# Kernel optimization log

Hardware: AMD Instinct MI355X
Metric: run time of the kernel (lower is better)

The kernel has to match this reference:

```python
import jax, jax.numpy as jnp
import numpy as np

D, H = 1024, 2048
N_STEPS = 2
T0, T1 = 0.0, 1.0


def setup_inputs() -> dict:
    key = jax.random.key(0)
    ks = jax.random.split(key, 5)
    s_in = 1.0 / np.sqrt(D)
    s_h = 1.0 / np.sqrt(H)
    return {
        "x0": jax.random.normal(ks[0], (D,), jnp.float32),
        "W1": jax.random.normal(ks[1], (D, H), jnp.float32) * s_in,
        "b1": jnp.zeros((H,), jnp.float32),
        "wt": jax.random.normal(ks[2], (H,), jnp.float32) * 0.1,
        "W2": jax.random.normal(ks[3], (H, H), jnp.float32) * s_h,
        "b2": jnp.zeros((H,), jnp.float32),
        "W3": jax.random.normal(ks[4], (H, D), jnp.float32) * s_h,
        "b3": jnp.zeros((D,), jnp.float32),
    }


def reference(x0, W1, b1, wt, W2, b2, W3, b3):
    dtype = x0.dtype

    def velocity(t, x):
        # 3-layer tanh MLP velocity field with additive time embedding
        h1 = jnp.tanh(x @ W1 + b1 + t * wt)
        h2 = jnp.tanh(h1 @ W2 + b2)
        return h2 @ W3 + b3

    def vel_and_div(t, x):
        # Mirror of _compute_velocity_and_divergence: linearize + vmap(jvp)
        # over identity to get the full Jacobian, then take its trace.
        v, jvp_fun = jax.linearize(lambda z: velocity(t, z), x)
        cols = jax.vmap(jvp_fun)(jnp.eye(D, dtype=dtype))  # [D, D]
        return v, jnp.trace(cols)

    def aug_dyn(t, x):
        v, div = vel_and_div(t, x)
        return v, -div  # (dx/dt, dlogq/dt)

    # Standard-normal base distribution log_prob at x0
    log2pi = jnp.log(jnp.asarray(2.0 * np.pi, dtype=dtype))
    logq0 = -0.5 * jnp.sum(x0 * x0) - 0.5 * D * log2pi

    dt = jnp.asarray((T1 - T0) / N_STEPS, dtype=dtype)

    def rk4_step(carry, i):
        x, logq = carry
        t = T0 + i * dt
        v1, dl1 = aug_dyn(t, x)
        v2, dl2 = aug_dyn(t + 0.5 * dt, x + 0.5 * dt * v1)
        v3, dl3 = aug_dyn(t + 0.5 * dt, x + 0.5 * dt * v2)
        v4, dl4 = aug_dyn(t + dt, x + dt * v3)
        x_new = x + (dt / 6.0) * (v1 + 2.0 * v2 + 2.0 * v3 + v4)
        logq_new = logq + (dt / 6.0) * (dl1 + 2.0 * dl2 + 2.0 * dl3 + dl4)
        return (x_new, logq_new), None

    (x1, logq1), _ = jax.lax.scan(
        rk4_step, (x0, logq0), jnp.arange(N_STEPS, dtype=dtype)
    )
    # concat [x1 (D,), logq1 ()] -> (D+1,) for a single output array
    return jnp.concatenate([x1, logq1[None]])
```

## Files before the change

### kernel.cpp

```cpp
#include <hip/hip_runtime.h>
#include <math.h>

#define DD 1024
#define HH 2048
#define NCB 256

typedef float f32x4 __attribute__((ext_vector_type(4)));
typedef short short8 __attribute__((ext_vector_type(8)));

__device__ __forceinline__ float b2f(unsigned short u) {
    return __uint_as_float(((unsigned int)u) << 16);
}
__device__ __forceinline__ unsigned short f2b(float f) {
    unsigned int x = __float_as_uint(f);
    unsigned int r = (x + 0x7FFFu + ((x >> 16) & 1u)) >> 16;
    return (unsigned short)r;
}
__device__ __forceinline__ float ald(const float* p) {
    return __hip_atomic_load(p, __ATOMIC_RELAXED, __HIP_MEMORY_SCOPE_AGENT);
}
__device__ __forceinline__ void ast(float* p, float v) {
    __hip_atomic_store(p, v, __ATOMIC_RELAXED, __HIP_MEMORY_SCOPE_AGENT);
}

__global__ __launch_bounds__(256) void k_preW1(const float* __restrict__ W1,
                                               unsigned short* __restrict__ W1T,
                                               unsigned* __restrict__ sync) {
    __shared__ float tile[64][65];
    const int b = blockIdx.x, t = threadIdx.x;
    if (b == 0) {
        #pragma unroll
        for (int q = 0; q < 19; ++q) {
            int i = t + q * 256;
            if (i < 4624) sync[i] = 0u;
        }
    }
    const int bx = b & 31, by = b >> 5;
    const int c0 = bx * 64, r0 = by * 64;
    const int cc = t & 63, rb = t >> 6;
    #pragma unroll
    for (int p = 0; p < 16; ++p) {
        int rr = p * 4 + rb;
        tile[rr][cc] = W1[(size_t)(r0 + rr) * HH + c0 + cc];
    }
    __syncthreads();
    #pragma unroll
    for (int p = 0; p < 16; ++p) {
        int rr = p * 4 + rb;
        W1T[(size_t)(c0 + rr) * DD + r0 + cc] = f2b(tile[cc][rr]);
    }
}

__global__ __launch_bounds__(256) void k_gemmPT(const unsigned short* __restrict__ W1T,
                                                const float* __restrict__ W2,
                                                const float* __restrict__ W3,
                                                const float* __restrict__ b3,
                                                const float* __restrict__ x0,
                                                unsigned short* __restrict__ Mb,
                                                unsigned short* __restrict__ Pb,
                                                unsigned short* __restrict__ W2T,
                                                unsigned short* __restrict__ W3T,
                                                float* __restrict__ c1,
                                                float* __restrict__ A1g) {
    const int b = blockIdx.x, t = threadIdx.x;
    if (b >= 256) {
        __shared__ float tile[64][65];
        int bb = b - 256;
        const float* in; unsigned short* out; int R, C, bx, by;
        if (bb < 1024) { in = W2; out = W2T; R = HH; C = HH; bx = bb & 31; by = bb >> 5; }
        else           { bb -= 1024; in = W3; out = W3T; R = HH; C = DD; bx = bb & 15; by = bb >> 4; }
        const int c0 = bx * 64, r0 = by * 64;
        const int cc = t & 63, rb = t >> 6;
        #pragma unroll
        for (int p = 0; p < 16; ++p) {
            int rr = p * 4 + rb;
            tile[rr][cc] = in[(size_t)(r0 + rr) * C + c0 + cc];
        }
        __syncthreads();
        #pragma unroll
        for (int p = 0; p < 16; ++p) {
            int rr = p * 4 + rb;
            out[(size_t)(c0 + rr) * R + r0 + cc] = f2b(tile[cc][rr]);
        }
        return;
    }
    __shared__ unsigned short At[128][40];
    __shared__ unsigned short Bt[128][40];
    const int m0 = (b >> 4) * 128;
    const int k0 = (b & 15) * 128;
    const int r = t & 127, half = t >> 7;
    const int wv = t >> 6, l = t & 63;
    const int wr = wv >> 1, wc = wv & 1;
    const int fr = l & 15, fg = l >> 4;
    const bool do_c1 = ((b & 15) == 0) && (t < 128);
    float c1acc = 0.f, a1acc = 0.f;

    f32x4 acc[4][4] = {};
    for (int i0 = 0; i0 < DD; i0 += 32) {
        {
            const float4* sa = (const float4*)(W1T + (size_t)(m0 + r) * DD + i0 + half * 16);
            float4 a0 = sa[0], a1 = sa[1];
            const float4* sbf = (const float4*)(W3 + (size_t)(k0 + r) * DD + i0 + half * 16);
            float4 f0 = sbf[0], f1 = sbf[1], f2v = sbf[2], f3 = sbf[3];
            float4* da = (float4*)&At[r][half * 16];
            da[0] = a0; da[1] = a1;
            short8 o0, o1;
            o0[0] = (short)f2b(f0.x); o0[1] = (short)f2b(f0.y); o0[2] = (short)f2b(f0.z); o0[3] = (short)f2b(f0.w);
            o0[4] = (short)f2b(f1.x); o0[5] = (short)f2b(f1.y); o0[6] = (short)f2b(f1.z); o0[7] = (short)f2b(f1.w);
            o1[0] = (short)f2b(f2v.x); o1[1] = (short)f2b(f2v.y); o1[2] = (short)f2b(f2v.z); o1[3] = (short)f2b(f2v.w);
            o1[4] = (short)f2b(f3.x); o1[5] = (short)f2b(f3.y); o1[6] = (short)f2b(f3.z); o1[7] = (short)f2b(f3.w);
            *(short8*)&Bt[r][half * 16] = o0;
            *(short8*)&Bt[r][half * 16 + 8] = o1;
        }
        __syncthreads();
        if (do_c1) {
            #pragma unroll
            for (int i = 0; i < 32; ++i) {
                float w1v = b2f(At[t][i]);
                c1acc += w1v * b3[i0 + i];
                a1acc += w1v * x0[i0 + i];
            }
        }
        short8 af[4], bf[4];
        #pragma unroll
        for (int a = 0; a < 4; ++a)
            af[a] = *(const short8*)&At[wr * 64 + a * 16 + fr][fg * 8];
        #pragma unroll
        for (int bq = 0; bq < 4; ++bq)
            bf[bq] = *(const short8*)&Bt[wc * 64 + bq * 16 + fr][fg * 8];
        #pragma unroll
        for (int a = 0; a < 4; ++a)
            #pragma unroll
            for (int bq = 0; bq < 4; ++bq)
                acc[a][bq] = __builtin_amdgcn_mfma_f32_16x16x32_bf16(af[a], bf[bq], acc[a][bq], 0, 0, 0);
        __syncthreads();
    }
    if (do_c1) { c1[m0 + t] = c1acc; A1g[m0 + t] = a1acc; }
    #pragma unroll
    for (int a = 0; a < 4; ++a) {
        #pragma unroll
        for (int bq = 0; bq < 4; ++bq) {
            #pragma unroll
            for (int j = 0; j < 4; ++j) {
                int row = m0 + wr * 64 + a * 16 + fg * 4 + j;
                int col = k0 + wc * 64 + bq * 16 + fr;
                size_t idx = (size_t)row * HH + col;
                float m = acc[a][bq][j];
                Mb[idx] = f2b(m);
                Pb[idx] = f2b(m * W2[idx]);
            }
        }
    }
}

__device__ __forceinline__ void gbar(unsigned* sync, int b, unsigned g) {
    __syncthreads();
    const int t = threadIdx.x;
    if (b == 0 && t >= 64 && t < 128) {
        const int l = t - 64;
        while (true) {
            bool ok = true;
            #pragma unroll
            for (int k = 0; k < 4; ++k) {
                unsigned f = __hip_atomic_load(&sync[(l + (k << 6)) << 4],
                                               __ATOMIC_RELAXED, __HIP_MEMORY_SCOPE_AGENT);
                ok &= (f >= g);
            }
            if (!__any((int)(!ok))) break;
            __builtin_amdgcn_s_sleep(1);
        }
        if (l < 16)
            __hip_atomic_store(&sync[4096 + (l << 4)], g, __ATOMIC_RELAXED, __HIP_MEMORY_SCOPE_AGENT);
    }
    if (t == 0) {
        asm volatile("s_waitcnt vmcnt(0)" ::: "memory");
        __hip_atomic_store(&sync[b << 4], g, __ATOMIC_RELAXED, __HIP_MEMORY_SCOPE_AGENT);
        while (__hip_atomic_load(&sync[4096 + ((b & 15) << 4)],
                                 __ATOMIC_RELAXED, __HIP_MEMORY_SCOPE_AGENT) < g)
            __builtin_amdgcn_s_sleep(2);
    }
    __syncthreads();
}

__global__ __launch_bounds__(256, 1) void k_chain(
    const unsigned short* __restrict__ Mb,
    const unsigned short* __restrict__ Pb,
    const unsigned short* __restrict__ W2T,
    const unsigned short* __restrict__ W3T,
    const float* __restrict__ x0,
    const float* __restrict__ b1, const float* __restrict__ wt,
    const float* __restrict__ b2, const float* __restrict__ b3,
    const float* __restrict__ c1, const float* __restrict__ A1g,
    float* __restrict__ h1_g, float* __restrict__ h2_g, float* __restrict__ hacc_g,
    float* __restrict__ out,
    unsigned* __restrict__ sync) {
    __shared__ unsigned short Ms[8][2048];
    __shared__ unsigned short Ps[8][2048];
    __shared__ unsigned short Qs[8][2048];
    __shared__ float vecH[2048];
    __shared__ float vecW[2048];
    __shared__ float wred[4];
    const int t = threadIdx.x, b = blockIdx.x;
    const int wib = t >> 6, lane = t & 63;
    const int gw2 = (b << 3) + (wib << 1);
    const int jx = (b << 2) + wib;
    unsigned g = 0;

    {
        const unsigned short* mp = Mb + (size_t)gw2 * HH;
        const unsigned short* pp = Pb + (size_t)gw2 * HH;
        const unsigned short* qp = W2T + (size_t)gw2 * HH;
        #pragma unroll
        for (int rep = 0; rep < 4; ++rep) {
            const int idx = rep * 512 + lane * 8;
            *(short8*)&Ms[wib * 2][idx]     = *(const short8*)(mp + idx);
            *(short8*)&Ms[wib * 2 + 1][idx] = *(const short8*)(mp + HH + idx);
            *(short8*)&Ps[wib * 2][idx]     = *(const short8*)(pp + idx);
            *(short8*)&Ps[wib * 2 + 1][idx] = *(const short8*)(pp + HH + idx);
            *(short8*)&Qs[wib * 2][idx]     = *(const short8*)(qp + idx);
            *(short8*)&Qs[wib * 2 + 1][idx] = *(const short8*)(qp + HH + idx);
        }
    }

    const float bb1_0 = b1[gw2], bb1_1 = b1[gw2 + 1];
    const float wt_0 = wt[gw2], wt_1 = wt[gw2 + 1];
    const float bb2_0 = b2[gw2], bb2_1 = b2[gw2 + 1];
    const float c1_0 = c1[gw2], c1_1 = c1[gw2 + 1];

    float A1_0 = 0.f, A1_1 = 0.f;
    float u0 = 0.f, u1 = 0.f;
    float hc0 = 0.f, hc1 = 0.f;
    float wdiv = 0.f;

    float logq_r = 0.f;
    if (b == 0 && wib == 0) {
        float ssum = 0.f;
        #pragma unroll
        for (int q = 0; q < 16; ++q) { float xv = x0[lane + (q << 6)]; ssum += xv * xv; }
        #pragma unroll
        for (int o = 1; o < 64; o <<= 1) ssum += __shfl_xor(ssum, o, 64);
        logq_r = -0.5f * ssum - 0.5f * 1024.0f * 1.8378770664093453f;
    }

    for (int s = 0; s < 8; ++s) {
        const int ss = s & 3;
        const float tcur = (s >> 2) * 0.5f + ((ss == 0) ? 0.f : (ss == 3) ? 0.5f : 0.25f);

        if (s == 0) {
            A1_0 = A1g[gw2]; A1_1 = A1g[gw2 + 1];
            float h0 = tanhf(A1_0 + bb1_0 + tcur * wt_0);
            float h1v = tanhf(A1_1 + bb1_1 + tcur * wt_1);
            u0 = 1.f - h0 * h0; u1 = 1.f - h1v * h1v;
            if (lane == 0) { ast(h1_g + gw2, h0); ast(h1_g + gw2 + 1, h1v); }
        } else {
            #pragma unroll
            for (int q = 0; q < 8; ++q) {
                int i = t + (q << 8);
                float h2v = ald(h2_g + i);
                float sv = (ss == 0) ? ald(hacc_g + i) : h2v;
                vecH[i] = sv;
                vecW[i] = 1.f - h2v * h2v;
            }
            __syncthreads();
            float md0 = 0.f, md1 = 0.f, pd0 = 0.f, pd1 = 0.f;
            #pragma unroll
            for (int rep = 0; rep < 4; ++rep) {
                const int idx = rep * 512 + lane * 8;
                float4 hA = *(const float4*)(vecH + idx);
                float4 hB = *(const float4*)(vecH + idx + 4);
                float4 wA = *(const float4*)(vecW + idx);
                float4 wB = *(const float4*)(vecW + idx + 4);
                float hv[8] = {hA.x, hA.y, hA.z, hA.w, hB.x, hB.y, hB.z, hB.w};
                float wv[8] = {wA.x, wA.y, wA.z, wA.w, wB.x, wB.y, wB.z, wB.w};
                short8 m0v = *(const short8*)&Ms[wib * 2][idx];
                short8 m1v = *(const short8*)&Ms[wib * 2 + 1][idx];
                short8 p0v = *(const short8*)&Ps[wib * 2][idx];
                short8 p1v = *(const short8*)&Ps[wib * 2 + 1][idx];
                #pragma unroll
                for (int e = 0; e < 8; ++e) {
                    md0 += b2f((unsigned short)m0v[e]) * hv[e];
                    md1 += b2f((unsigned short)m1v[e]) * hv[e];
                    pd0 += b2f((unsigned short)p0v[e]) * wv[e];
                    pd1 += b2f((unsigned short)p1v[e]) * wv[e];
                }
            }
            #pragma unroll
            for (int o = 1; o < 64; o <<= 1) {
                md0 += __shfl_xor(md0, o, 64); md1 += __shfl_xor(md1, o, 64);
                pd0 += __shfl_xor(pd0, o, 64); pd1 += __shfl_xor(pd1, o, 64);
            }
            const int sp = (s - 1) & 3;
            const float cprev = (sp == 1 || sp == 2) ? (1.f / 6.f) : (1.f / 12.f);
            wdiv += cprev * (u0 * pd0 + u1 * pd1);
            float pre0, pre1;
            if (ss == 0) {
                A1_0 += md0 + 0.5f * c1_0; A1_1 += md1 + 0.5f * c1_1;
                pre0 = A1_0 + bb1_0 + tcur * wt_0; pre1 = A1_1 + bb1_1 + tcur * wt_1;
            } else {
                const float a = (ss == 3) ? 0.5f : 0.25f;
                pre0 = A1_0 + a * (md0 + c1_0) + bb1_0 + tcur * wt_0;
                pre1 = A1_1 + a * (md1 + c1_1) + bb1_1 + tcur * wt_1;
            }
            float h0 = tanhf(pre0), h1v = tanhf(pre1);
            u0 = 1.f - h0 * h0; u1 = 1.f - h1v * h1v;
            if (lane == 0) { ast(h1_g + gw2, h0); ast(h1_g + gw2 + 1, h1v); }
        }
        gbar(sync, b, ++g);

        #pragma unroll
        for (int q = 0; q < 8; ++q) {
            int i = t + (q << 8);
            vecH[i] = ald(h1_g + i);
        }
        __syncthreads();
        {
            float a0 = 0.f, a1 = 0.f;
            #pragma unroll
            for (int rep = 0; rep < 4; ++rep) {
                const int idx = rep * 512 + lane * 8;
                float4 hA = *(const float4*)(vecH + idx);
                float4 hB = *(const float4*)(vecH + idx + 4);
                float hv[8] = {hA.x, hA.y, hA.z, hA.w, hB.x, hB.y, hB.z, hB.w};
                short8 r0 = *(const short8*)&Qs[wib * 2][idx];
                short8 r1 = *(const short8*)&Qs[wib * 2 + 1][idx];
                #pragma unroll
                for (int e = 0; e < 8; ++e) {
                    a0 += b2f((unsigned short)r0[e]) * hv[e];
                    a1 += b2f((unsigned short)r1[e]) * hv[e];
                }
            }
            #pragma unroll
            for (int o = 1; o < 64; o <<= 1) {
                a0 += __shfl_xor(a0, o, 64); a1 += __shfl_xor(a1, o, 64);
            }
            float q0 = tanhf(a0 + bb2_0), q1 = tanhf(a1 + bb2_1);
            const float cs = (ss == 1 || ss == 2) ? (1.f / 6.f) : (1.f / 12.f);
            hc0 += cs * q0; hc1 += cs * q1;
            if (lane == 0) {
                ast(h2_g + gw2, q0); ast(h2_g + gw2 + 1, q1);
                if (ss == 3) { ast(hacc_g + gw2, hc0); ast(hacc_g + gw2 + 1, hc1); }
            }
        }
        gbar(sync, b, ++g);
    }

    {
        #pragma unroll
        for (int q = 0; q < 8; ++q) {
            int i = t + (q << 8);
            float h2v = ald(h2_g + i);
            vecH[i] = ald(hacc_g + i);
            vecW[i] = 1.f - h2v * h2v;
        }
        __syncthreads();
        float pd0 = 0.f, pd1 = 0.f, xo = 0.f;
        const unsigned short* Vr = W3T + (size_t)jx * HH;
        #pragma unroll
        for (int rep = 0; rep < 4; ++rep) {
            const int idx = rep * 512 + lane * 8;
            float4 cA = *(const float4*)(vecH + idx);
            float4 cB = *(const float4*)(vecH + idx + 4);
            float4 wA = *(const float4*)(vecW + idx);
            float4 wB = *(const float4*)(vecW + idx + 4);
            float cv[8] = {cA.x, cA.y, cA.z, cA.w, cB.x, cB.y, cB.z, cB.w};
            float wv[8] = {wA.x, wA.y, wA.z, wA.w, wB.x, wB.y, wB.z, wB.w};
            short8 p0v = *(const short8*)&Ps[wib * 2][idx];
            short8 p1v = *(const short8*)&Ps[wib * 2 + 1][idx];
            short8 vv = *(const short8*)(Vr + idx);
            #pragma unroll
            for (int e = 0; e < 8; ++e) {
                pd0 += b2f((unsigned short)p0v[e]) * wv[e];
                pd1 += b2f((unsigned short)p1v[e]) * wv[e];
                xo  += b2f((unsigned short)vv[e]) * cv[e];
            }
        }
        #pragma unroll
        for (int o = 1; o < 64; o <<= 1) {
            pd0 += __shfl_xor(pd0, o, 64); pd1 += __shfl_xor(pd1, o, 64);
            xo += __shfl_xor(xo, o, 64);
        }
        wdiv += (1.f / 12.f) * (u0 * pd0 + u1 * pd1);
        if (lane == 0) {
            out[jx] = x0[jx] + xo + b3[jx];
            wred[wib] = wdiv;
        }
    }
    __syncthreads();
    if (t == 0) {
        float dsum = wred[0] + wred[1] + wred[2] + wred[3];
        atomicAdd((float*)(sync + 4352 + (b & 15) * 16), dsum);
        asm volatile("s_waitcnt vmcnt(0)" ::: "memory");
        atomicAdd(sync + 4608, 1u);
    }
    if (b == 0 && wib == 0) {
        if (lane < 16) {
            while (__hip_atomic_load(sync + 4608, __ATOMIC_RELAXED, __HIP_MEMORY_SCOPE_AGENT) < NCB)
                __builtin_amdgcn_s_sleep(2);
        }
        float v = 0.f;
        if (lane < 16) {
            unsigned du = __hip_atomic_load(sync + 4352 + lane * 16,
                                            __ATOMIC_RELAXED, __HIP_MEMORY_SCOPE_AGENT);
            v = __uint_as_float(du);
        }
        #pragma unroll
        for (int o = 1; o < 64; o <<= 1) v += __shfl_xor(v, o, 64);
        if (lane == 0) out[DD] = logq_r - v;
    }
}

extern "C" void kernel_launch(void* const* d_in, const int* in_sizes, int n_in,
                              void* d_out, int out_size, void* d_ws, size_t ws_size,
                              hipStream_t stream) {
    const float* x0 = (const float*)d_in[0];
    const float* W1 = (const float*)d_in[1];
    const float* b1 = (const float*)d_in[2];
    const float* wt = (const float*)d_in[3];
    const float* W2 = (const float*)d_in[4];
    const float* b2 = (const float*)d_in[5];
    const float* W3 = (const float*)d_in[6];
    const float* b3 = (const float*)d_in[7];
    float* out = (float*)d_out;

    char* ws = (char*)d_ws;
    const size_t MB = 1024 * 1024;
    unsigned short* Pb  = (unsigned short*)(ws);
    unsigned short* W1T = (unsigned short*)(ws + 8 * MB);
    unsigned short* W2T = (unsigned short*)(ws + 12 * MB);
    unsigned short* W3T = (unsigned short*)(ws + 20 * MB);
    unsigned short* Mb  = (unsigned short*)(ws + 24 * MB);
    float* fb = (float*)(ws + 32 * MB);
    float* h1_g    = fb;
    float* h2_g    = fb + 2048;
    float* hacc_g  = fb + 4096;
    float* c1      = fb + 6144;
    float* A1g     = fb + 8192;
    unsigned* sync = (unsigned*)(fb + 10240);

    k_preW1<<<512, 256, 0, stream>>>(W1, W1T, sync);
    k_gemmPT<<<1792, 256, 0, stream>>>(W1T, W2, W3, b3, x0, Mb, Pb, W2T, W3T, c1, A1g);
    k_chain<<<NCB, 256, 0, stream>>>(Mb, Pb, W2T, W3T, x0, b1, wt, b2, b3, c1, A1g,
                                     h1_g, h2_g, hacc_g, out, sync);
}
```

Baseline: 167.9 us.

## Replace global barriers with tagged per-element dataflow sync and fuse W1 transpose

Removes the centralized grid barrier in the chain kernel and instead packs each published hidden value with a 32-bit step tag in a 64-bit word. Consumers spin only until the specific elements they need carry a sufficient tag. This eliminates the two full-grid barriers per stage. Separately, the W1 pre-transpose kernel is dropped: the GEMM reads W1 column-wise directly with strided loads and converts to bf16 in place, saving a launch and a pass over W1. Tile indexing is swapped so the aux dot products run in the first row of blocks. Risks are more polling traffic, 64-bit atomic loads, and uncoalesced strided W1 reads.

Result: slower. 177.2 us (+5.5%).

```diff
diff --git a/kernel.cpp b/kernel.cpp
--- a/kernel.cpp
+++ b/kernel.cpp
@@ -7,6 +7,7 @@
 
 typedef float f32x4 __attribute__((ext_vector_type(4)));
 typedef short short8 __attribute__((ext_vector_type(8)));
+typedef unsigned long long ull;
 
 __device__ __forceinline__ float b2f(unsigned short u) {
     return __uint_as_float(((unsigned int)u) << 16);
@@ -16,42 +17,20 @@
     unsigned int r = (x + 0x7FFFu + ((x >> 16) & 1u)) >> 16;
     return (unsigned short)r;
 }
-__device__ __forceinline__ float ald(const float* p) {
+__device__ __forceinline__ ull ald64(const ull* p) {
     return __hip_atomic_load(p, __ATOMIC_RELAXED, __HIP_MEMORY_SCOPE_AGENT);
 }
-__device__ __forceinline__ void ast(float* p, float v) {
+__device__ __forceinline__ void ast64(ull* p, ull v) {
     __hip_atomic_store(p, v, __ATOMIC_RELAXED, __HIP_MEMORY_SCOPE_AGENT);
 }
-
-__global__ __launch_bounds__(256) void k_preW1(const float* __restrict__ W1,
-                                               unsigned short* __restrict__ W1T,
-                                               unsigned* __restrict__ sync) {
-    __shared__ float tile[64][65];
-    const int b = blockIdx.x, t = threadIdx.x;
-    if (b == 0) {
-        #pragma unroll
-        for (int q = 0; q < 19; ++q) {
-            int i = t + q * 256;
-            if (i < 4624) sync[i] = 0u;
-        }
-    }
-    const int bx = b & 31, by = b >> 5;
-    const int c0 = bx * 64, r0 = by * 64;
-    const int cc = t & 63, rb = t >> 6;
-    #pragma unroll
-    for (int p = 0; p < 16; ++p) {
-        int rr = p * 4 + rb;
-        tile[rr][cc] = W1[(size_t)(r0 + rr) * HH + c0 + cc];
-    }
-    __syncthreads();
-    #pragma unroll
-    for (int p = 0; p < 16; ++p) {
-        int rr = p * 4 + rb;
-        W1T[(size_t)(c0 + rr) * DD + r0 + cc] = f2b(tile[cc][rr]);
-    }
-}
-
-__global__ __launch_bounds__(256) void k_gemmPT(const unsigned short* __restrict__ W1T,
+__device__ __forceinline__ ull pkh(float h, unsigned g) {
+    return ((ull)g << 32) | (ull)(unsigned)__float_as_uint(h);
+}
+__device__ __forceinline__ float loh(ull v) {
+    return __uint_as_float((unsigned)v);
+}
+
+__global__ __launch_bounds__(256) void k_gemmPT(const float* __restrict__ W1,
                                                 const float* __restrict__ W2,
                                                 const float* __restrict__ W3,
                                                 const float* __restrict__ b3,
@@ -61,11 +40,19 @@
                                                 unsigned short* __restrict__ W2T,
                                                 unsigned short* __restrict__ W3T,
                                                 float* __restrict__ c1,
-                                                float* __restrict__ A1g) {
+                                                float* __restrict__ A1g,
+                                                float* __restrict__ h1t,
+                                                float* __restrict__ h2t,
+                                                float* __restrict__ hacct,
+                                                unsigned* __restrict__ sync) {
     const int b = blockIdx.x, t = threadIdx.x;
     if (b >= 256) {
+        int bb = b - 256;
+        if (bb == 0) { float4 z = make_float4(0, 0, 0, 0); for (int q = 0; q < 4; ++q) ((float4*)h1t)[t * 4 + q] = z; }
+        else if (bb == 1) { float4 z = make_float4(0, 0, 0, 0); for (int q = 0; q < 4; ++q) ((float4*)h2t)[t * 4 + q] = z; }
+        else if (bb == 2) { float4 z = make_float4(0, 0, 0, 0); for (int q = 0; q < 4; ++q) ((float4*)hacct)[t * 4 + q] = z; }
+        else if (bb == 3) { if (t < 512) sync[t] = 0u; }
         __shared__ float tile[64][65];
-        int bb = b - 256;
         const float* in; unsigned short* out; int R, C, bx, by;
         if (bb < 1024) { in = W2; out = W2T; R = HH; C = HH; bx = bb & 31; by = bb >> 5; }
         else           { bb -= 1024; in = W3; out = W3T; R = HH; C = DD; bx = bb & 15; by = bb >> 4; }
@@ -86,24 +73,31 @@
     }
     __shared__ unsigned short At[128][40];
     __shared__ unsigned short Bt[128][40];
-    const int m0 = (b >> 4) * 128;
-    const int k0 = (b & 15) * 128;
+    const int m0 = (b & 15) * 128;
+    const int k0 = (b >> 4) * 128;
     const int r = t & 127, half = t >> 7;
     const int wv = t >> 6, l = t & 63;
     const int wr = wv >> 1, wc = wv & 1;
     const int fr = l & 15, fg = l >> 4;
-    const bool do_c1 = ((b & 15) == 0) && (t < 128);
+    const bool do_aux = ((b >> 4) == 0) && (t < 128);
     float c1acc = 0.f, a1acc = 0.f;
 
     f32x4 acc[4][4] = {};
     for (int i0 = 0; i0 < DD; i0 += 32) {
         {
-            const float4* sa = (const float4*)(W1T + (size_t)(m0 + r) * DD + i0 + half * 16);
-            float4 a0 = sa[0], a1 = sa[1];
+            const float* wp = W1 + (size_t)(i0 + half * 16) * HH + m0 + r;
+            float v[16];
+            #pragma unroll
+            for (int k2 = 0; k2 < 16; ++k2) v[k2] = wp[(size_t)k2 * HH];
+            short8 o0, o1;
+            #pragma unroll
+            for (int e = 0; e < 8; ++e) { o0[e] = (short)f2b(v[e]); o1[e] = (short)f2b(v[8 + e]); }
+            *(short8*)&At[r][half * 16] = o0;
+            *(short8*)&At[r][half * 16 + 8] = o1;
+        }
+        {
             const float4* sbf = (const float4*)(W3 + (size_t)(k0 + r) * DD + i0 + half * 16);
             float4 f0 = sbf[0], f1 = sbf[1], f2v = sbf[2], f3 = sbf[3];
-            float4* da = (float4*)&At[r][half * 16];
-            da[0] = a0; da[1] = a1;
             short8 o0, o1;
             o0[0] = (short)f2b(f0.x); o0[1] = (short)f2b(f0.y); o0[2] = (short)f2b(f0.z); o0[3] = (short)f2b(f0.w);
             o0[4] = (short)f2b(f1.x); o0[5] = (short)f2b(f1.y); o0[6] = (short)f2b(f1.z); o0[7] = (short)f2b(f1.w);
@@ -113,7 +107,7 @@
             *(short8*)&Bt[r][half * 16 + 8] = o1;
         }
         __syncthreads();
-        if (do_c1) {
+        if (do_aux) {
             #pragma unroll
             for (int i = 0; i < 32; ++i) {
                 float w1v = b2f(At[t][i]);
@@ -135,7 +129,7 @@
                 acc[a][bq] = __builtin_amdgcn_mfma_f32_16x16x32_bf16(af[a], bf[bq], acc[a][bq], 0, 0, 0);
         __syncthreads();
     }
-    if (do_c1) { c1[m0 + t] = c1acc; A1g[m0 + t] = a1acc; }
+    if (do_aux) { c1[m0 + t] = c1acc; A1g[m0 + t] = a1acc; }
     #pragma unroll
     for (int a = 0; a < 4; ++a) {
         #pragma unroll
@@ -151,35 +145,6 @@
             }
         }
     }
-}
-
-__device__ __forceinline__ void gbar(unsigned* sync, int b, unsigned g) {
-    __syncthreads();
-    const int t = threadIdx.x;
-    if (b == 0 && t >= 64 && t < 128) {
-        const int l = t - 64;
-        while (true) {
-            bool ok = true;
-            #pragma unroll
-            for (int k = 0; k < 4; ++k) {
-                unsigned f = __hip_atomic_load(&sync[(l + (k << 6)) << 4],
-                                               __ATOMIC_RELAXED, __HIP_MEMORY_SCOPE_AGENT);
-                ok &= (f >= g);
-            }
-            if (!__any((int)(!ok))) break;
-            __builtin_amdgcn_s_sleep(1);
-        }
-        if (l < 16)
-            __hip_atomic_store(&sync[4096 + (l << 4)], g, __ATOMIC_RELAXED, __HIP_MEMORY_SCOPE_AGENT);
-    }
-    if (t == 0) {
-        asm volatile("s_waitcnt vmcnt(0)" ::: "memory");
-        __hip_atomic_store(&sync[b << 4], g, __ATOMIC_RELAXED, __HIP_MEMORY_SCOPE_AGENT);
-        while (__hip_atomic_load(&sync[4096 + ((b & 15) << 4)],
-                                 __ATOMIC_RELAXED, __HIP_MEMORY_SCOPE_AGENT) < g)
-            __builtin_amdgcn_s_sleep(2);
-    }
-    __syncthreads();
 }
 
 __global__ __launch_bounds__(256, 1) void k_chain(
@@ -191,7 +156,7 @@
     const float* __restrict__ b1, const float* __restrict__ wt,
     const float* __restrict__ b2, const float* __restrict__ b3,
     const float* __restrict__ c1, const float* __restrict__ A1g,
-    float* __restrict__ h1_g, float* __restrict__ h2_g, float* __restrict__ hacc_g,
+    ull* __restrict__ h1t, ull* __restrict__ h2t, ull* __restrict__ hacct,
     float* __restrict__ out,
     unsigned* __restrict__ sync) {
     __shared__ unsigned short Ms[8][2048];
@@ -204,7 +169,6 @@
     const int wib = t >> 6, lane = t & 63;
     const int gw2 = (b << 3) + (wib << 1);
     const int jx = (b << 2) + wib;
-    unsigned g = 0;
 
     {
         const unsigned short* mp = Mb + (size_t)gw2 * HH;
@@ -245,21 +209,45 @@
     for (int s = 0; s < 8; ++s) {
         const int ss = s & 3;
         const float tcur = (s >> 2) * 0.5f + ((ss == 0) ? 0.f : (ss == 3) ? 0.5f : 0.25f);
+        const unsigned tagA = 2 * s + 1;
+        const unsigned tagB = 2 * s + 2;
 
         if (s == 0) {
             A1_0 = A1g[gw2]; A1_1 = A1g[gw2 + 1];
             float h0 = tanhf(A1_0 + bb1_0 + tcur * wt_0);
             float h1v = tanhf(A1_1 + bb1_1 + tcur * wt_1);
             u0 = 1.f - h0 * h0; u1 = 1.f - h1v * h1v;
-            if (lane == 0) { ast(h1_g + gw2, h0); ast(h1_g + gw2 + 1, h1v); }
+            if (lane == 0) { ast64(h1t + gw2, pkh(h0, tagA)); ast64(h1t + gw2 + 1, pkh(h1v, tagA)); }
         } else {
-            #pragma unroll
-            for (int q = 0; q < 8; ++q) {
-                int i = t + (q << 8);
-                float h2v = ald(h2_g + i);
-                float sv = (ss == 0) ? ald(hacc_g + i) : h2v;
-                vecH[i] = sv;
-                vecW[i] = 1.f - h2v * h2v;
+            const unsigned need = 2 * s;
+            ull va[8];
+            #pragma unroll
+            for (int q = 0; q < 8; ++q) va[q] = ald64(h2t + t + (q << 8));
+            #pragma unroll
+            for (int q = 0; q < 8; ++q)
+                while ((unsigned)(va[q] >> 32) < need) { __builtin_amdgcn_s_sleep(1); va[q] = ald64(h2t + t + (q << 8)); }
+            if (ss == 0) {
+                ull vb[8];
+                #pragma unroll
+                for (int q = 0; q < 8; ++q) vb[q] = ald64(hacct + t + (q << 8));
+                #pragma unroll
+                for (int q = 0; q < 8; ++q)
+                    while ((unsigned)(vb[q] >> 32) < need) { __builtin_amdgcn_s_sleep(1); vb[q] = ald64(hacct + t + (q << 8)); }
+                #pragma unroll
+                for (int q = 0; q < 8; ++q) {
+                    int i = t + (q << 8);
+                    float h2v = loh(va[q]);
+                    vecW[i] = 1.f - h2v * h2v;
+                    vecH[i] = loh(vb[q]);
+                }
+            } else {
+                #pragma unroll
+                for (int q = 0; q < 8; ++q) {
+                    int i = t + (q << 8);
+                    float h2v = loh(va[q]);
+                    vecW[i] = 1.f - h2v * h2v;
+                    vecH[i] = h2v;
+                }
             }
             __syncthreads();
             float md0 = 0.f, md1 = 0.f, pd0 = 0.f, pd1 = 0.f;
@@ -303,14 +291,18 @@
             }
             float h0 = tanhf(pre0), h1v = tanhf(pre1);
             u0 = 1.f - h0 * h0; u1 = 1.f - h1v * h1v;
-            if (lane == 0) { ast(h1_g + gw2, h0); ast(h1_g + gw2 + 1, h1v); }
-        }
-        gbar(sync, b, ++g);
-
-        #pragma unroll
-        for (int q = 0; q < 8; ++q) {
-            int i = t + (q << 8);
-            vecH[i] = ald(h1_g + i);
+            if (lane == 0) { ast64(h1t + gw2, pkh(h0, tagA)); ast64(h1t + gw2 + 1, pkh(h1v, tagA)); }
+        }
+
+        {
+            ull va[8];
+            #pragma unroll
+            for (int q = 0; q < 8; ++q) va[q] = ald64(h1t + t + (q << 8));
+            #pragma unroll
+            for (int q = 0; q < 8; ++q)
+                while ((unsigned)(va[q] >> 32) < tagA) { __builtin_amdgcn_s_sleep(1); va[q] = ald64(h1t + t + (q << 8)); }
+            #pragma unroll
+            for (int q = 0; q < 8; ++q) vecH[t + (q << 8)] = loh(va[q]);
         }
         __syncthreads();
         {
@@ -337,20 +329,32 @@
             const float cs = (ss == 1 || ss == 2) ? (1.f / 6.f) : (1.f / 12.f);
             hc0 += cs * q0; hc1 += cs * q1;
             if (lane == 0) {
-                ast(h2_g + gw2, q0); ast(h2_g + gw2 + 1, q1);
-                if (ss == 3) { ast(hacc_g + gw2, hc0); ast(hacc_g + gw2 + 1, hc1); }
-            }
-        }
-        gbar(sync, b, ++g);
+                if (ss == 3) {
+                    ast64(hacct + gw2, pkh(hc0, tagB));
+                    ast64(hacct + gw2 + 1, pkh(hc1, tagB));
+                }
+                ast64(h2t + gw2, pkh(q0, tagB));
+                ast64(h2t + gw2 + 1, pkh(q1, tagB));
+            }
+        }
+        __syncthreads();
     }
 
     {
+        ull va[8], vb[8];
+        #pragma unroll
+        for (int q = 0; q < 8; ++q) { va[q] = ald64(h2t + t + (q << 8)); vb[q] = ald64(hacct + t + (q << 8)); }
+        #pragma unroll
+        for (int q = 0; q < 8; ++q) {
+            while ((unsigned)(va[q] >> 32) < 16u) { __builtin_amdgcn_s_sleep(1); va[q] = ald64(h2t + t + (q << 8)); }
+            while ((unsigned)(vb[q] >> 32) < 16u) { __builtin_amdgcn_s_sleep(1); vb[q] = ald64(hacct + t + (q << 8)); }
+        }
         #pragma unroll
         for (int q = 0; q < 8; ++q) {
             int i = t + (q << 8);
-            float h2v = ald(h2_g + i);
-            vecH[i] = ald(hacc_g + i);
+            float h2v = loh(va[q]);
             vecW[i] = 1.f - h2v * h2v;
+            vecH[i] = loh(vb[q]);
         }
         __syncthreads();
         float pd0 = 0.f, pd1 = 0.f, xo = 0.f;
@@ -388,19 +392,19 @@
     __syncthreads();
     if (t == 0) {
         float dsum = wred[0] + wred[1] + wred[2] + wred[3];
-        atomicAdd((float*)(sync + 4352 + (b & 15) * 16), dsum);
+        atomicAdd((float*)(sync + (b & 15) * 16), dsum);
         asm volatile("s_waitcnt vmcnt(0)" ::: "memory");
-        atomicAdd(sync + 4608, 1u);
+        atomicAdd(sync + 256, 1u);
     }
     if (b == 0 && wib == 0) {
-        if (lane < 16) {
-            while (__hip_atomic_load(sync + 4608, __ATOMIC_RELAXED, __HIP_MEMORY_SCOPE_AGENT) < NCB)
+        if (lane == 0) {
+            while (__hip_atomic_load(sync + 256, __ATOMIC_RELAXED, __HIP_MEMORY_SCOPE_AGENT) < NCB)
                 __builtin_amdgcn_s_sleep(2);
         }
+        __syncthreads();
         float v = 0.f;
         if (lane < 16) {
-            unsigned du = __hip_atomic_load(sync + 4352 + lane * 16,
-                                            __ATOMIC_RELAXED, __HIP_MEMORY_SCOPE_AGENT);
+            unsigned du = __hip_atomic_load(sync + lane * 16, __ATOMIC_RELAXED, __HIP_MEMORY_SCOPE_AGENT);
             v = __uint_as_float(du);
         }
         #pragma unroll
@@ -425,20 +429,19 @@
     char* ws = (char*)d_ws;
     const size_t MB = 1024 * 1024;
     unsigned short* Pb  = (unsigned short*)(ws);
-    unsigned short* W1T = (unsigned short*)(ws + 8 * MB);
-    unsigned short* W2T = (unsigned short*)(ws + 12 * MB);
-    unsigned short* W3T = (unsigned short*)(ws + 20 * MB);
-    unsigned short* Mb  = (unsigned short*)(ws + 24 * MB);
-    float* fb = (float*)(ws + 32 * MB);
-    float* h1_g    = fb;
-    float* h2_g    = fb + 2048;
-    float* hacc_g  = fb + 4096;
-    float* c1      = fb + 6144;
-    float* A1g     = fb + 8192;
-    unsigned* sync = (unsigned*)(fb + 10240);
-
-    k_preW1<<<512, 256, 0, stream>>>(W1, W1T, sync);
-    k_gemmPT<<<1792, 256, 0, stream>>>(W1T, W2, W3, b3, x0, Mb, Pb, W2T, W3T, c1, A1g);
+    unsigned short* W2T = (unsigned short*)(ws + 8 * MB);
+    unsigned short* W3T = (unsigned short*)(ws + 16 * MB);
+    unsigned short* Mb  = (unsigned short*)(ws + 20 * MB);
+    float* fb = (float*)(ws + 28 * MB);
+    float* c1      = fb;
+    float* A1g     = fb + 2048;
+    ull* h1t       = (ull*)(fb + 4096);
+    ull* h2t       = (ull*)(fb + 8192);
+    ull* hacct     = (ull*)(fb + 12288);
+    unsigned* sync = (unsigned*)(fb + 16384);
+
+    k_gemmPT<<<1792, 256, 0, stream>>>(W1, W2, W3, b3, x0, Mb, Pb, W2T, W3T,
+                                       c1, A1g, (float*)h1t, (float*)h2t, (float*)hacct, sync);
     k_chain<<<NCB, 256, 0, stream>>>(Mb, Pb, W2T, W3T, x0, b1, wt, b2, b3, c1, A1g,
-                                     h1_g, h2_g, hacc_g, out, sync);
-}
+                                     h1t, h2t, hacct, out, sync);
+}
```

## Fuse W1 transpose into GEMM prologue and flatten grid barrier

Applied to the files above, without the earlier changes.

Removes the separate W1 transpose kernel. The GEMM now reads W1 directly with strided column loads and converts it to bf16 while staging it into shared memory, and sync-buffer zeroing moves into one of the GEMM's transpose blocks. The grid barrier drops the two-level master/release scheme: every block now polls all arrival flags itself. This saves a kernel launch and a round trip through the intermediate buffer. The cost is uncoalesced-looking strided W1 loads, redundant W1 reads across the 16 k-tiles, and more polling traffic on the flags.

Result: slower. 173.5 us (+3.3%).

```diff
diff --git a/kernel.cpp b/kernel.cpp
--- a/kernel.cpp
+++ b/kernel.cpp
@@ -23,35 +23,7 @@
     __hip_atomic_store(p, v, __ATOMIC_RELAXED, __HIP_MEMORY_SCOPE_AGENT);
 }
 
-__global__ __launch_bounds__(256) void k_preW1(const float* __restrict__ W1,
-                                               unsigned short* __restrict__ W1T,
-                                               unsigned* __restrict__ sync) {
-    __shared__ float tile[64][65];
-    const int b = blockIdx.x, t = threadIdx.x;
-    if (b == 0) {
-        #pragma unroll
-        for (int q = 0; q < 19; ++q) {
-            int i = t + q * 256;
-            if (i < 4624) sync[i] = 0u;
-        }
-    }
-    const int bx = b & 31, by = b >> 5;
-    const int c0 = bx * 64, r0 = by * 64;
-    const int cc = t & 63, rb = t >> 6;
-    #pragma unroll
-    for (int p = 0; p < 16; ++p) {
-        int rr = p * 4 + rb;
-        tile[rr][cc] = W1[(size_t)(r0 + rr) * HH + c0 + cc];
-    }
-    __syncthreads();
-    #pragma unroll
-    for (int p = 0; p < 16; ++p) {
-        int rr = p * 4 + rb;
-        W1T[(size_t)(c0 + rr) * DD + r0 + cc] = f2b(tile[cc][rr]);
-    }
-}
-
-__global__ __launch_bounds__(256) void k_gemmPT(const unsigned short* __restrict__ W1T,
+__global__ __launch_bounds__(256) void k_gemmPT(const float* __restrict__ W1,
                                                 const float* __restrict__ W2,
                                                 const float* __restrict__ W3,
                                                 const float* __restrict__ b3,
@@ -61,11 +33,19 @@
                                                 unsigned short* __restrict__ W2T,
                                                 unsigned short* __restrict__ W3T,
                                                 float* __restrict__ c1,
-                                                float* __restrict__ A1g) {
+                                                float* __restrict__ A1g,
+                                                unsigned* __restrict__ sync) {
     const int b = blockIdx.x, t = threadIdx.x;
     if (b >= 256) {
+        int bb = b - 256;
+        if (bb == 0) {
+            #pragma unroll
+            for (int q = 0; q < 18; ++q) {
+                int i = t + q * 256;
+                if (i < 4368) sync[i] = 0u;
+            }
+        }
         __shared__ float tile[64][65];
-        int bb = b - 256;
         const float* in; unsigned short* out; int R, C, bx, by;
         if (bb < 1024) { in = W2; out = W2T; R = HH; C = HH; bx = bb & 31; by = bb >> 5; }
         else           { bb -= 1024; in = W3; out = W3T; R = HH; C = DD; bx = bb & 15; by = bb >> 4; }
@@ -86,24 +66,31 @@
     }
     __shared__ unsigned short At[128][40];
     __shared__ unsigned short Bt[128][40];
-    const int m0 = (b >> 4) * 128;
-    const int k0 = (b & 15) * 128;
+    const int m0 = (b & 15) * 128;
+    const int k0 = (b >> 4) * 128;
     const int r = t & 127, half = t >> 7;
     const int wv = t >> 6, l = t & 63;
     const int wr = wv >> 1, wc = wv & 1;
     const int fr = l & 15, fg = l >> 4;
-    const bool do_c1 = ((b & 15) == 0) && (t < 128);
+    const bool do_aux = ((b >> 4) == 0) && (t < 128);
     float c1acc = 0.f, a1acc = 0.f;
 
     f32x4 acc[4][4] = {};
     for (int i0 = 0; i0 < DD; i0 += 32) {
         {
-            const float4* sa = (const float4*)(W1T + (size_t)(m0 + r) * DD + i0 + half * 16);
-            float4 a0 = sa[0], a1 = sa[1];
+            const float* wp = W1 + (size_t)(i0 + half * 16) * HH + m0 + r;
+            float v[16];
+            #pragma unroll
+            for (int k2 = 0; k2 < 16; ++k2) v[k2] = wp[(size_t)k2 * HH];
+            short8 o0, o1;
+            #pragma unroll
+            for (int e = 0; e < 8; ++e) { o0[e] = (short)f2b(v[e]); o1[e] = (short)f2b(v[8 + e]); }
+            *(short8*)&At[r][half * 16] = o0;
+            *(short8*)&At[r][half * 16 + 8] = o1;
+        }
+        {
             const float4* sbf = (const float4*)(W3 + (size_t)(k0 + r) * DD + i0 + half * 16);
             float4 f0 = sbf[0], f1 = sbf[1], f2v = sbf[2], f3 = sbf[3];
-            float4* da = (float4*)&At[r][half * 16];
-            da[0] = a0; da[1] = a1;
             short8 o0, o1;
             o0[0] = (short)f2b(f0.x); o0[1] = (short)f2b(f0.y); o0[2] = (short)f2b(f0.z); o0[3] = (short)f2b(f0.w);
             o0[4] = (short)f2b(f1.x); o0[5] = (short)f2b(f1.y); o0[6] = (short)f2b(f1.z); o0[7] = (short)f2b(f1.w);
@@ -113,7 +100,7 @@
             *(short8*)&Bt[r][half * 16 + 8] = o1;
         }
         __syncthreads();
-        if (do_c1) {
+        if (do_aux) {
             #pragma unroll
             for (int i = 0; i < 32; ++i) {
                 float w1v = b2f(At[t][i]);
@@ -135,7 +122,7 @@
                 acc[a][bq] = __builtin_amdgcn_mfma_f32_16x16x32_bf16(af[a], bf[bq], acc[a][bq], 0, 0, 0);
         __syncthreads();
     }
-    if (do_c1) { c1[m0 + t] = c1acc; A1g[m0 + t] = a1acc; }
+    if (do_aux) { c1[m0 + t] = c1acc; A1g[m0 + t] = a1acc; }
     #pragma unroll
     for (int a = 0; a < 4; ++a) {
         #pragma unroll
@@ -155,29 +142,22 @@
 
 __device__ __forceinline__ void gbar(unsigned* sync, int b, unsigned g) {
     __syncthreads();
-    const int t = threadIdx.x;
-    if (b == 0 && t >= 64 && t < 128) {
-        const int l = t - 64;
+    if (threadIdx.x < 64) {
+        if (threadIdx.x == 0) {
+            asm volatile("s_waitcnt vmcnt(0)" ::: "memory");
+            __hip_atomic_store(&sync[b << 4], g, __ATOMIC_RELAXED, __HIP_MEMORY_SCOPE_AGENT);
+        }
         while (true) {
             bool ok = true;
             #pragma unroll
             for (int k = 0; k < 4; ++k) {
-                unsigned f = __hip_atomic_load(&sync[(l + (k << 6)) << 4],
+                unsigned f = __hip_atomic_load(&sync[(threadIdx.x + (k << 6)) << 4],
                                                __ATOMIC_RELAXED, __HIP_MEMORY_SCOPE_AGENT);
                 ok &= (f >= g);
             }
             if (!__any((int)(!ok))) break;
             __builtin_amdgcn_s_sleep(1);
         }
-        if (l < 16)
-            __hip_atomic_store(&sync[4096 + (l << 4)], g, __ATOMIC_RELAXED, __HIP_MEMORY_SCOPE_AGENT);
-    }
-    if (t == 0) {
-        asm volatile("s_waitcnt vmcnt(0)" ::: "memory");
-        __hip_atomic_store(&sync[b << 4], g, __ATOMIC_RELAXED, __HIP_MEMORY_SCOPE_AGENT);
-        while (__hip_atomic_load(&sync[4096 + ((b & 15) << 4)],
-                                 __ATOMIC_RELAXED, __HIP_MEMORY_SCOPE_AGENT) < g)
-            __builtin_amdgcn_s_sleep(2);
     }
     __syncthreads();
 }
@@ -388,18 +368,18 @@
     __syncthreads();
     if (t == 0) {
         float dsum = wred[0] + wred[1] + wred[2] + wred[3];
-        atomicAdd((float*)(sync + 4352 + (b & 15) * 16), dsum);
+        atomicAdd((float*)(sync + 4096 + (b & 15) * 16), dsum);
         asm volatile("s_waitcnt vmcnt(0)" ::: "memory");
-        atomicAdd(sync + 4608, 1u);
+        atomicAdd(sync + 4352, 1u);
     }
     if (b == 0 && wib == 0) {
-        if (lane < 16) {
-            while (__hip_atomic_load(sync + 4608, __ATOMIC_RELAXED, __HIP_MEMORY_SCOPE_AGENT) < NCB)
+        if (lane == 0) {
+            while (__hip_atomic_load(sync + 4352, __ATOMIC_RELAXED, __HIP_MEMORY_SCOPE_AGENT) < NCB)
                 __builtin_amdgcn_s_sleep(2);
         }
         float v = 0.f;
         if (lane < 16) {
-            unsigned du = __hip_atomic_load(sync + 4352 + lane * 16,
+            unsigned du = __hip_atomic_load(sync + 4096 + lane * 16,
                                             __ATOMIC_RELAXED, __HIP_MEMORY_SCOPE_AGENT);
             v = __uint_as_float(du);
         }
@@ -425,20 +405,19 @@
     char* ws = (char*)d_ws;
     const size_t MB = 1024 * 1024;
     unsigned short* Pb  = (unsigned short*)(ws);
-    unsigned short* W1T = (unsigned short*)(ws + 8 * MB);
-    unsigned short* W2T = (unsigned short*)(ws + 12 * MB);
-    unsigned short* W3T = (unsigned short*)(ws + 20 * MB);
-    unsigned short* Mb  = (unsigned short*)(ws + 24 * MB);
-    float* fb = (float*)(ws + 32 * MB);
-    float* h1_g    = fb;
-    float* h2_g    = fb + 2048;
-    float* hacc_g  = fb + 4096;
-    float* c1      = fb + 6144;
-    float* A1g     = fb + 8192;
+    unsigned short* W2T = (unsigned short*)(ws + 8 * MB);
+    unsigned short* W3T = (unsigned short*)(ws + 16 * MB);
+    unsigned short* Mb  = (unsigned short*)(ws + 20 * MB);
+    float* fb = (float*)(ws + 28 * MB);
+    float* c1      = fb;
+    float* A1g     = fb + 2048;
+    float* h1_g    = fb + 4096;
+    float* h2_g    = fb + 6144;
+    float* hacc_g  = fb + 8192;
     unsigned* sync = (unsigned*)(fb + 10240);
 
-    k_preW1<<<512, 256, 0, stream>>>(W1, W1T, sync);
-    k_gemmPT<<<1792, 256, 0, stream>>>(W1T, W2, W3, b3, x0, Mb, Pb, W2T, W3T, c1, A1g);
+    k_gemmPT<<<1792, 256, 0, stream>>>(W1, W2, W3, b3, x0, Mb, Pb, W2T, W3T,
+                                       c1, A1g, sync);
     k_chain<<<NCB, 256, 0, stream>>>(Mb, Pb, W2T, W3T, x0, b1, wt, b2, b3, c1, A1g,
                                      h1_g, h2_g, hacc_g, out, sync);
 }
```
